# Kernel optimization log

Measured on AMD Instinct MI355X. Metric: run time of the kernel, lower is better.

## Reference

```python
import jax, jax.numpy as jnp
import numpy as np

B, IN_DIM, OUT_DIM, DEGREE = 512, 256, 256, 5
SCALE = 0.5 / (DEGREE + 1)


def setup_inputs() -> dict:
    key = jax.random.key(0)
    k1, k2, k3 = jax.random.split(key, 3)
    x = jax.random.normal(k1, (B, IN_DIM), dtype=jnp.float32)
    slopes = jnp.arange(DEGREE + 1, dtype=jnp.float32)
    weights_p = jax.random.normal(k2, (IN_DIM, OUT_DIM, DEGREE + 1), dtype=jnp.float32) * SCALE
    weights_q = jax.random.normal(k3, (IN_DIM, OUT_DIM, DEGREE + 1), dtype=jnp.float32) * SCALE
    return {"x": x, "slopes": slopes, "weights_p": weights_p, "weights_q": weights_q}


def reference(x, slopes, weights_p, weights_q):
    # Training-mode forward (temp = 1.0): logsumexp over degree axis.
    # lin: (B, in_dim, 1, degree+1)
    lin = x[:, :, None, None] * slopes
    # broadcast with (in_dim, out_dim, degree+1) -> (B, in_dim, out_dim, degree+1)
    p_val = jax.nn.logsumexp(lin + weights_p, axis=-1)  # (B, in_dim, out_dim)
    q_val = jax.nn.logsumexp(lin + weights_q, axis=-1)  # (B, in_dim, out_dim)
    return jnp.sum(p_val - q_val, axis=1)  # (B, out_dim)
```

## Files before the change

### kernel.cpp

```cpp
#include <hip/hip_runtime.h>
#include <math.h>

#define BATCH   512
#define IN_DIM  256
#define OUT_DIM 256

#define OT     8
#define NSEG   32
#define ISEG   8
#define NB     32

#define PRESCALE 12.476649250079015f

__launch_bounds__(256, 4)
__global__ void tropical_fused(const float* __restrict__ x,
                               const float* __restrict__ wp,
                               const float* __restrict__ wq,
                               float* __restrict__ out) {
    __shared__ float lds[NSEG * (NB * OT + 1)];

    const int tid = threadIdx.x;
    const int o_l = tid & (OT - 1);
    const int b0  = blockIdx.y * NB;

    {
        const int r0 = tid >> 4;
        const int c  = (tid & 15) * 16;
#pragma unroll
        for (int p = 0; p < 2; ++p) {
            const int r = p * 16 + r0;
            const float* xr = x + (size_t)(b0 + r) * IN_DIM + c;
#pragma unroll
            for (int q = 0; q < 4; ++q) {
                const float4 v = *(const float4*)(xr + q * 4);
                float4 w;
                w.x = __expf(v.x); w.y = __expf(v.y);
                w.z = __expf(v.z); w.w = __expf(v.w);
                *(float4*)&lds[r * IN_DIM + c + q * 4] = w;
            }
        }
    }
    __syncthreads();

    float acc[NB];
#pragma unroll
    for (int b = 0; b < NB; ++b) acc[b] = 0.f;

    const int seg    = tid >> 3;
    const int i_base = seg * ISEG;
    const int o      = blockIdx.x * OT + o_l;
    const float* __restrict__ tb = lds + i_base;

#pragma unroll
    for (int g = 0; g < 2; ++g) {
        float cp[4][6], cq[4][6];
#pragma unroll
        for (int ii = 0; ii < 4; ++ii) {
            const int j = (i_base + g * 4 + ii) * OUT_DIM + o;
            const float2* P2 = (const float2*)wp + (size_t)j * 3;
            const float2* Q2 = (const float2*)wq + (size_t)j * 3;
            const float2 p0 = P2[0], p1 = P2[1], p2 = P2[2];
            const float2 q0 = Q2[0], q1 = Q2[1], q2 = Q2[2];
            cp[ii][0] = __expf(p0.x - PRESCALE);
            cp[ii][1] = __expf(p0.y - PRESCALE);
            cp[ii][2] = __expf(p1.x - PRESCALE);
            cp[ii][3] = __expf(p1.y - PRESCALE);
            cp[ii][4] = __expf(p2.x - PRESCALE);
            cp[ii][5] = __expf(p2.y - PRESCALE);
            cq[ii][0] = __expf(q0.x - PRESCALE);
            cq[ii][1] = __expf(q0.y - PRESCALE);
            cq[ii][2] = __expf(q1.x - PRESCALE);
            cq[ii][3] = __expf(q1.y - PRESCALE);
            cq[ii][4] = __expf(q2.x - PRESCALE);
            cq[ii][5] = __expf(q2.y - PRESCALE);
        }

#pragma unroll
        for (int b = 0; b < NB; ++b) {
            const float4 tv = *(const float4*)(tb + b * IN_DIM + g * 4);
            const float t0 = tv.x, t1 = tv.y, t2 = tv.z, t3 = tv.w;

            float P0 = fmaf(fmaf(fmaf(fmaf(fmaf(cp[0][5], t0, cp[0][4]),
                         t0, cp[0][3]), t0, cp[0][2]), t0, cp[0][1]), t0, cp[0][0]);
            float P1 = fmaf(fmaf(fmaf(fmaf(fmaf(cp[1][5], t1, cp[1][4]),
                         t1, cp[1][3]), t1, cp[1][2]), t1, cp[1][1]), t1, cp[1][0]);
            float P2v = fmaf(fmaf(fmaf(fmaf(fmaf(cp[2][5], t2, cp[2][4]),
                         t2, cp[2][3]), t2, cp[2][2]), t2, cp[2][1]), t2, cp[2][0]);
            float P3 = fmaf(fmaf(fmaf(fmaf(fmaf(cp[3][5], t3, cp[3][4]),
                         t3, cp[3][3]), t3, cp[3][2]), t3, cp[3][1]), t3, cp[3][0]);

            float Q0 = fmaf(fmaf(fmaf(fmaf(fmaf(cq[0][5], t0, cq[0][4]),
                         t0, cq[0][3]), t0, cq[0][2]), t0, cq[0][1]), t0, cq[0][0]);
            float Q1 = fmaf(fmaf(fmaf(fmaf(fmaf(cq[1][5], t1, cq[1][4]),
                         t1, cq[1][3]), t1, cq[1][2]), t1, cq[1][1]), t1, cq[1][0]);
            float Q2v = fmaf(fmaf(fmaf(fmaf(fmaf(cq[2][5], t2, cq[2][4]),
                         t2, cq[2][3]), t2, cq[2][2]), t2, cq[2][1]), t2, cq[2][0]);
            float Q3 = fmaf(fmaf(fmaf(fmaf(fmaf(cq[3][5], t3, cq[3][4]),
                         t3, cq[3][3]), t3, cq[3][2]), t3, cq[3][1]), t3, cq[3][0]);

            const float mp = (P0 * P1) * (P2v * P3);
            const float mq = (Q0 * Q1) * (Q2v * Q3);
            acc[b] += __log2f(mp) - __log2f(mq);
        }
    }

    __syncthreads();
#pragma unroll
    for (int b = 0; b < NB; ++b)
        lds[seg * (NB * OT + 1) + b * OT + o_l] = acc[b];
    __syncthreads();

    {
        const int br  = tid >> 3;
        const int orr = tid & (OT - 1);
        float s = 0.f;
#pragma unroll
        for (int g2 = 0; g2 < NSEG; ++g2)
            s += lds[g2 * (NB * OT + 1) + br * OT + orr];
        out[(size_t)(b0 + br) * OUT_DIM + blockIdx.x * OT + orr] =
            s * 0.6931471805599453f;
    }
}

extern "C" void kernel_launch(void* const* d_in, const int* in_sizes, int n_in,
                              void* d_out, int out_size, void* d_ws, size_t ws_size,
                              hipStream_t stream) {
    const float* x  = (const float*)d_in[0];
    const float* wp = (const float*)d_in[2];
    const float* wq = (const float*)d_in[3];
    float* out = (float*)d_out;

    dim3 grid(OUT_DIM / OT, BATCH / NB);
    tropical_fused<<<grid, 256, 0, stream>>>(x, wp, wq, out);
}
```

Baseline: 20.28 us.

## Halve batch tile per block and hoist first weight load before x staging

Reduces the batch rows per block from 32 to 16, doubling the grid to 1024 blocks and halving the per-thread accumulator array, which should ease register pressure and improve occupancy and load balance across CUs. It also issues the first group of weight loads and exponentials before staging x into LDS, so global weight latency overlaps the x load. The trade-off is that each block now recomputes the weight exponentials for half as much batch work, doubling total weight reads and exp work, and half the threads sit idle in the final reduction.

```diff
diff --git a/kernel.cpp b/kernel.cpp
--- a/kernel.cpp
+++ b/kernel.cpp
@@ -8,7 +8,7 @@
 #define OT     8
 #define NSEG   32
 #define ISEG   8
-#define NB     32
+#define NB     16
 
 #define PRESCALE 12.476649250079015f
 
@@ -23,21 +23,43 @@
     const int o_l = tid & (OT - 1);
     const int b0  = blockIdx.y * NB;
 
+    const int seg    = tid >> 3;
+    const int i_base = seg * ISEG;
+    const int o      = blockIdx.x * OT + o_l;
+
+    float cp[4][6], cq[4][6];
+#pragma unroll
+    for (int ii = 0; ii < 4; ++ii) {
+        const int j = (i_base + ii) * OUT_DIM + o;
+        const float2* P2 = (const float2*)wp + (size_t)j * 3;
+        const float2* Q2 = (const float2*)wq + (size_t)j * 3;
+        const float2 p0 = P2[0], p1 = P2[1], p2 = P2[2];
+        const float2 q0 = Q2[0], q1 = Q2[1], q2 = Q2[2];
+        cp[ii][0] = __expf(p0.x - PRESCALE);
+        cp[ii][1] = __expf(p0.y - PRESCALE);
+        cp[ii][2] = __expf(p1.x - PRESCALE);
+        cp[ii][3] = __expf(p1.y - PRESCALE);
+        cp[ii][4] = __expf(p2.x - PRESCALE);
+        cp[ii][5] = __expf(p2.y - PRESCALE);
+        cq[ii][0] = __expf(q0.x - PRESCALE);
+        cq[ii][1] = __expf(q0.y - PRESCALE);
+        cq[ii][2] = __expf(q1.x - PRESCALE);
+        cq[ii][3] = __expf(q1.y - PRESCALE);
+        cq[ii][4] = __expf(q2.x - PRESCALE);
+        cq[ii][5] = __expf(q2.y - PRESCALE);
+    }
+
     {
-        const int r0 = tid >> 4;
-        const int c  = (tid & 15) * 16;
+        const int r = tid >> 4;
+        const int c = (tid & 15) * 16;
+        const float* xr = x + (size_t)(b0 + r) * IN_DIM + c;
 #pragma unroll
-        for (int p = 0; p < 2; ++p) {
-            const int r = p * 16 + r0;
-            const float* xr = x + (size_t)(b0 + r) * IN_DIM + c;
-#pragma unroll
-            for (int q = 0; q < 4; ++q) {
-                const float4 v = *(const float4*)(xr + q * 4);
-                float4 w;
-                w.x = __expf(v.x); w.y = __expf(v.y);
-                w.z = __expf(v.z); w.w = __expf(v.w);
-                *(float4*)&lds[r * IN_DIM + c + q * 4] = w;
-            }
+        for (int q = 0; q < 4; ++q) {
+            const float4 v = *(const float4*)(xr + q * 4);
+            float4 w;
+            w.x = __expf(v.x); w.y = __expf(v.y);
+            w.z = __expf(v.z); w.w = __expf(v.w);
+            *(float4*)&lds[r * IN_DIM + c + q * 4] = w;
         }
     }
     __syncthreads();
@@ -46,33 +68,31 @@
 #pragma unroll
     for (int b = 0; b < NB; ++b) acc[b] = 0.f;
 
-    const int seg    = tid >> 3;
-    const int i_base = seg * ISEG;
-    const int o      = blockIdx.x * OT + o_l;
     const float* __restrict__ tb = lds + i_base;
 
 #pragma unroll
     for (int g = 0; g < 2; ++g) {
-        float cp[4][6], cq[4][6];
+        if (g == 1) {
 #pragma unroll
-        for (int ii = 0; ii < 4; ++ii) {
-            const int j = (i_base + g * 4 + ii) * OUT_DIM + o;
-            const float2* P2 = (const float2*)wp + (size_t)j * 3;
-            const float2* Q2 = (const float2*)wq + (size_t)j * 3;
-            const float2 p0 = P2[0], p1 = P2[1], p2 = P2[2];
-            const float2 q0 = Q2[0], q1 = Q2[1], q2 = Q2[2];
-            cp[ii][0] = __expf(p0.x - PRESCALE);
-            cp[ii][1] = __expf(p0.y - PRESCALE);
-            cp[ii][2] = __expf(p1.x - PRESCALE);
-            cp[ii][3] = __expf(p1.y - PRESCALE);
-            cp[ii][4] = __expf(p2.x - PRESCALE);
-            cp[ii][5] = __expf(p2.y - PRESCALE);
-            cq[ii][0] = __expf(q0.x - PRESCALE);
-            cq[ii][1] = __expf(q0.y - PRESCALE);
-            cq[ii][2] = __expf(q1.x - PRESCALE);
-            cq[ii][3] = __expf(q1.y - PRESCALE);
-            cq[ii][4] = __expf(q2.x - PRESCALE);
-            cq[ii][5] = __expf(q2.y - PRESCALE);
+            for (int ii = 0; ii < 4; ++ii) {
+                const int j = (i_base + 4 + ii) * OUT_DIM + o;
+                const float2* P2 = (const float2*)wp + (size_t)j * 3;
+                const float2* Q2 = (const float2*)wq + (size_t)j * 3;
+                const float2 p0 = P2[0], p1 = P2[1], p2 = P2[2];
+                const float2 q0 = Q2[0], q1 = Q2[1], q2 = Q2[2];
+                cp[ii][0] = __expf(p0.x - PRESCALE);
+                cp[ii][1] = __expf(p0.y - PRESCALE);
+                cp[ii][2] = __expf(p1.x - PRESCALE);
+                cp[ii][3] = __expf(p1.y - PRESCALE);
+                cp[ii][4] = __expf(p2.x - PRESCALE);
+                cp[ii][5] = __expf(p2.y - PRESCALE);
+                cq[ii][0] = __expf(q0.x - PRESCALE);
+                cq[ii][1] = __expf(q0.y - PRESCALE);
+                cq[ii][2] = __expf(q1.x - PRESCALE);
+                cq[ii][3] = __expf(q1.y - PRESCALE);
+                cq[ii][4] = __expf(q2.x - PRESCALE);
+                cq[ii][5] = __expf(q2.y - PRESCALE);
+            }
         }
 
 #pragma unroll
@@ -80,23 +100,23 @@
             const float4 tv = *(const float4*)(tb + b * IN_DIM + g * 4);
             const float t0 = tv.x, t1 = tv.y, t2 = tv.z, t3 = tv.w;
 
-            float P0 = fmaf(fmaf(fmaf(fmaf(fmaf(cp[0][5], t0, cp[0][4]),
-                         t0, cp[0][3]), t0, cp[0][2]), t0, cp[0][1]), t0, cp[0][0]);
-            float P1 = fmaf(fmaf(fmaf(fmaf(fmaf(cp[1][5], t1, cp[1][4]),
-                         t1, cp[1][3]), t1, cp[1][2]), t1, cp[1][1]), t1, cp[1][0]);
-            float P2v = fmaf(fmaf(fmaf(fmaf(fmaf(cp[2][5], t2, cp[2][4]),
-                         t2, cp[2][3]), t2, cp[2][2]), t2, cp[2][1]), t2, cp[2][0]);
-            float P3 = fmaf(fmaf(fmaf(fmaf(fmaf(cp[3][5], t3, cp[3][4]),
-                         t3, cp[3][3]), t3, cp[3][2]), t3, cp[3][1]), t3, cp[3][0]);
+            const float P0 = fmaf(fmaf(fmaf(fmaf(fmaf(cp[0][5], t0, cp[0][4]),
+                t0, cp[0][3]), t0, cp[0][2]), t0, cp[0][1]), t0, cp[0][0]);
+            const float P1 = fmaf(fmaf(fmaf(fmaf(fmaf(cp[1][5], t1, cp[1][4]),
+                t1, cp[1][3]), t1, cp[1][2]), t1, cp[1][1]), t1, cp[1][0]);
+            const float P2v = fmaf(fmaf(fmaf(fmaf(fmaf(cp[2][5], t2, cp[2][4]),
+                t2, cp[2][3]), t2, cp[2][2]), t2, cp[2][1]), t2, cp[2][0]);
+            const float P3 = fmaf(fmaf(fmaf(fmaf(fmaf(cp[3][5], t3, cp[3][4]),
+                t3, cp[3][3]), t3, cp[3][2]), t3, cp[3][1]), t3, cp[3][0]);
 
-            float Q0 = fmaf(fmaf(fmaf(fmaf(fmaf(cq[0][5], t0, cq[0][4]),
-                         t0, cq[0][3]), t0, cq[0][2]), t0, cq[0][1]), t0, cq[0][0]);
-            float Q1 = fmaf(fmaf(fmaf(fmaf(fmaf(cq[1][5], t1, cq[1][4]),
-                         t1, cq[1][3]), t1, cq[1][2]), t1, cq[1][1]), t1, cq[1][0]);
-            float Q2v = fmaf(fmaf(fmaf(fmaf(fmaf(cq[2][5], t2, cq[2][4]),
-                         t2, cq[2][3]), t2, cq[2][2]), t2, cq[2][1]), t2, cq[2][0]);
-            float Q3 = fmaf(fmaf(fmaf(fmaf(fmaf(cq[3][5], t3, cq[3][4]),
-                         t3, cq[3][3]), t3, cq[3][2]), t3, cq[3][1]), t3, cq[3][0]);
+            const float Q0 = fmaf(fmaf(fmaf(fmaf(fmaf(cq[0][5], t0, cq[0][4]),
+                t0, cq[0][3]), t0, cq[0][2]), t0, cq[0][1]), t0, cq[0][0]);
+            const float Q1 = fmaf(fmaf(fmaf(fmaf(fmaf(cq[1][5], t1, cq[1][4]),
+                t1, cq[1][3]), t1, cq[1][2]), t1, cq[1][1]), t1, cq[1][0]);
+            const float Q2v = fmaf(fmaf(fmaf(fmaf(fmaf(cq[2][5], t2, cq[2][4]),
+                t2, cq[2][3]), t2, cq[2][2]), t2, cq[2][1]), t2, cq[2][0]);
+            const float Q3 = fmaf(fmaf(fmaf(fmaf(fmaf(cq[3][5], t3, cq[3][4]),
+                t3, cq[3][3]), t3, cq[3][2]), t3, cq[3][1]), t3, cq[3][0]);
 
             const float mp = (P0 * P1) * (P2v * P3);
             const float mq = (Q0 * Q1) * (Q2v * Q3);
@@ -110,9 +130,8 @@
         lds[seg * (NB * OT + 1) + b * OT + o_l] = acc[b];
     __syncthreads();
 
-    {
-        const int br  = tid >> 3;
-        const int orr = tid & (OT - 1);
+    if (tid < NB * OT) {
+        const int br = tid >> 3, orr = tid & (OT - 1);
         float s = 0.f;
 #pragma unroll
         for (int g2 = 0; g2 < NSEG; ++g2)
```

Result: slower. 21.96 us (+8.3%).
